# Kernel optimization log

Measured on AMD Instinct MI355X. Metric: run time of the kernel, lower is better.

The kernel has to match this reference:

```python
import jax, jax.numpy as jnp
import numpy as np

B, T, S, D = 8, 64, 256, 512


def setup_inputs() -> dict:
    key = jax.random.key(0)
    ks = jax.random.split(key, 8)
    scale = 1.0 / np.sqrt(D)
    return {
        "source": jax.random.normal(ks[0], (B, T, D), jnp.float32),
        "memory_bank": jax.random.normal(ks[1], (B, S, D), jnp.float32),
        "source_masks": jnp.ones((B, T), jnp.float32),
        # params (torch Linear stored as [out,in]; here as [in,out] so y = x @ W + b)
        "Wq": jax.random.normal(ks[2], (D, D), jnp.float32) * scale,
        "bq": jnp.zeros((D,), jnp.float32),
        "Wv": jax.random.normal(ks[3], (D, D), jnp.float32) * scale,
        "Wc": jax.random.normal(ks[4], (2 * D, 2), jnp.float32) * scale,
        "bc": jnp.zeros((2,), jnp.float32),
    }


def reference(source, memory_bank, source_masks, Wq, bq, Wv, Wc, bc):
    # accumulate(): running mean over segments == cumsum / (1..T), then mask
    counts = jnp.arange(1, T + 1, dtype=source.dtype)  # [T]
    acc = jnp.cumsum(source, axis=1) / counts[None, :, None]  # [B,T,D]
    acc = acc * source_masks[:, :, None]

    # score(): h_t = linear_query(acc); gate = v(tanh(h_t + h_s)) broadcast over (t,s)
    ht = acc @ Wq + bq  # [B,T,D]
    gate = jnp.tanh(ht[:, :, None, :] + memory_bank[:, None, :, :]) @ Wv  # [B,T,S,D]
    sum_gate = gate.sum(axis=-1)  # [B,T,S]

    # linear_cate(cat([h_s, sum_gate*h_s], -1)) split as two [D,2] matmuls;
    # sum_gate is a per-(b,t,s) scalar so (sum_gate*h_s)@Wc2 == sum_gate*(h_s@Wc2).
    part1 = memory_bank @ Wc[:D]  # [B,S,2]
    part2 = memory_bank @ Wc[D:]  # [B,S,2]
    h_fuse = part1[:, None] + sum_gate[..., None] * part2[:, None] + bc  # [B,T,S,2]
    return h_fuse
```

## Files before the change

### kernel.cpp

```cpp
#include <hip/hip_runtime.h>

constexpr int B = 8, T = 64, S = 256, D = 512;
constexpr float SCL = 2.885390081777927f;

__global__ __launch_bounds__(256) void k_prep(const float* __restrict__ src,
                                              const float* __restrict__ mask,
                                              const float* __restrict__ Wv,
                                              const float* __restrict__ Wc,
                                              const float* __restrict__ bc,
                                              const float* __restrict__ mem,
                                              float* __restrict__ acc,
                                              float* __restrict__ wv,
                                              float* __restrict__ part1,
                                              float* __restrict__ part2) {
    const int blk = blockIdx.x;
    const int tid = threadIdx.x;
    if (blk < 16) {
        int idx = blk * 256 + tid;
        int b = idx >> 9, d = idx & (D - 1);
        const float* sp = src + (size_t)b * T * D + d;
        float v[T];
#pragma unroll
        for (int t = 0; t < T; ++t) v[t] = sp[(size_t)t * D];
        const float* mp = mask + b * T;
        float* ap = acc + (size_t)b * T * D + d;
        float run = 0.f;
#pragma unroll
        for (int t = 0; t < T; ++t) {
            run += v[t];
            ap[(size_t)t * D] = run * (1.0f / (float)(t + 1)) * mp[t];
        }
    } else if (blk < 144) {
        int row = (blk - 16) * 4 + (tid >> 6);
        int lane = tid & 63;
        const float* r = Wv + (size_t)row * D;
        float s = 0.f;
#pragma unroll
        for (int j = 0; j < D / 64; ++j) s += r[lane + j * 64];
#pragma unroll
        for (int off = 32; off; off >>= 1) s += __shfl_down(s, off);
        if (lane == 0) wv[row] = s;
    } else {
        int row = (blk - 144) * 4 + (tid >> 6);
        int lane = tid & 63;
        const float* mrow = mem + (size_t)row * D;
        float a0 = 0, a1 = 0, a2 = 0, a3 = 0;
        for (int d = lane; d < D; d += 64) {
            float m = mrow[d];
            float2 w1 = *(const float2*)(Wc + d * 2);
            float2 w2 = *(const float2*)(Wc + (D + d) * 2);
            a0 = fmaf(m, w1.x, a0); a1 = fmaf(m, w1.y, a1);
            a2 = fmaf(m, w2.x, a2); a3 = fmaf(m, w2.y, a3);
        }
#pragma unroll
        for (int off = 32; off; off >>= 1) {
            a0 += __shfl_down(a0, off);
            a1 += __shfl_down(a1, off);
            a2 += __shfl_down(a2, off);
            a3 += __shfl_down(a3, off);
        }
        if (lane == 0) {
            part1[row * 2 + 0] = a0 + bc[0];
            part1[row * 2 + 1] = a1 + bc[1];
            part2[row * 2 + 0] = a2;
            part2[row * 2 + 1] = a3;
        }
    }
}

__global__ __launch_bounds__(128) void k_ht(const float* __restrict__ acc,
                                            const float* __restrict__ Wq,
                                            const float* __restrict__ bq,
                                            float* __restrict__ ht) {
    __shared__ float AL[32][34];
    __shared__ float BL[32][36];
    const int tid = threadIdx.x;
    const int r0 = blockIdx.x * 32;
    const int c0 = blockIdx.y * 32;
    const int tx = tid & 7;
    const int ty = tid >> 3;
    float s00 = 0, s01 = 0, s02 = 0, s03 = 0, s10 = 0, s11 = 0, s12 = 0, s13 = 0;
    for (int d0 = 0; d0 < D; d0 += 32) {
        __syncthreads();
#pragma unroll
        for (int k = 0; k < 2; ++k) {
            int idx = tid + k * 128;
            int row = idx >> 3;
            int c4 = (idx & 7) * 4;
            float4 va = *(const float4*)(acc + (size_t)(r0 + row) * D + d0 + c4);
            AL[c4 + 0][row] = va.x; AL[c4 + 1][row] = va.y;
            AL[c4 + 2][row] = va.z; AL[c4 + 3][row] = va.w;
            float4 vb = *(const float4*)(Wq + (size_t)(d0 + row) * D + c0 + c4);
            *(float4*)&BL[row][c4] = vb;
        }
        __syncthreads();
#pragma unroll
        for (int dd = 0; dd < 32; ++dd) {
            float2 a = *(const float2*)&AL[dd][ty * 2];
            float4 bv = *(const float4*)&BL[dd][tx * 4];
            s00 = fmaf(a.x, bv.x, s00); s01 = fmaf(a.x, bv.y, s01);
            s02 = fmaf(a.x, bv.z, s02); s03 = fmaf(a.x, bv.w, s03);
            s10 = fmaf(a.y, bv.x, s10); s11 = fmaf(a.y, bv.y, s11);
            s12 = fmaf(a.y, bv.z, s12); s13 = fmaf(a.y, bv.w, s13);
        }
    }
    int r = r0 + ty * 2, c = c0 + tx * 4;
    float4 bqv = *(const float4*)(bq + c);
    *(float4*)(ht + (size_t)r * D + c) = make_float4(
        (s00 + bqv.x) * SCL, (s01 + bqv.y) * SCL, (s02 + bqv.z) * SCL, (s03 + bqv.w) * SCL);
    *(float4*)(ht + (size_t)(r + 1) * D + c) = make_float4(
        (s10 + bqv.x) * SCL, (s11 + bqv.y) * SCL, (s12 + bqv.z) * SCL, (s13 + bqv.w) * SCL);
}

__global__ __launch_bounds__(512) void k_fusepi(const float* __restrict__ ht,
                                                const float* __restrict__ mem,
                                                const float* __restrict__ wv,
                                                const float* __restrict__ part1,
                                                const float* __restrict__ part2,
                                                float* __restrict__ out) {
    __shared__ float htT[64][17];
    __shared__ float memT[64][34];
    __shared__ float wvL[64];
    const int tid = threadIdx.x;
    const int sb = blockIdx.x;
    const int tb = blockIdx.y;
    const int b  = blockIdx.z;
    const int st = tid & 31;
    const int tt = tid >> 5;
    const float* htBase  = ht  + ((size_t)b * T + tb * 16) * D;
    const float* memBase = mem + ((size_t)b * S + sb * 32) * D;
    float a = 0.f;
#pragma unroll 1
    for (int c = 0; c < 8; ++c) {
        const int d0 = c * 64;
        __syncthreads();
        {
            int row = tid >> 4;
            int c4 = (tid & 15) * 4;
            float4 v = *(const float4*)(memBase + (size_t)row * D + d0 + c4);
            memT[c4 + 0][row] = v.x * SCL; memT[c4 + 1][row] = v.y * SCL;
            memT[c4 + 2][row] = v.z * SCL; memT[c4 + 3][row] = v.w * SCL;
        }
        if (tid < 256) {
            int row = tid >> 4;
            int c4 = (tid & 15) * 4;
            float4 v = *(const float4*)(htBase + (size_t)row * D + d0 + c4);
            htT[c4 + 0][row] = v.x; htT[c4 + 1][row] = v.y;
            htT[c4 + 2][row] = v.z; htT[c4 + 3][row] = v.w;
        } else if (tid < 272) {
            int j = tid - 256;
            float4 v = *(const float4*)(wv + d0 + j * 4);
            wvL[j * 4 + 0] = v.x; wvL[j * 4 + 1] = v.y;
            wvL[j * 4 + 2] = v.z; wvL[j * 4 + 3] = v.w;
        }
        __syncthreads();
#pragma unroll 8
        for (int dd = 0; dd < 64; ++dd) {
            float x = htT[dd][tt] + memT[dd][st];
            float e = __builtin_amdgcn_exp2f(x);
            float r = __builtin_amdgcn_rcpf(e + 1.0f);
            float th = fmaf(-2.0f, r, 1.0f);
            a = fmaf(wvL[dd], th, a);
        }
    }
    const int t = tb * 16 + tt, s = sb * 32 + st;
    float2 p1 = *(const float2*)(part1 + ((size_t)b * S + s) * 2);
    float2 p2 = *(const float2*)(part2 + ((size_t)b * S + s) * 2);
    float* o = out + (((size_t)b * T + t) * S + s) * 2;
    *(float2*)o = make_float2(p1.x + a * p2.x, p1.y + a * p2.y);
}

extern "C" void kernel_launch(void* const* d_in, const int* in_sizes, int n_in,
                              void* d_out, int out_size, void* d_ws, size_t ws_size,
                              hipStream_t stream) {
    const float* source = (const float*)d_in[0];
    const float* memory = (const float*)d_in[1];
    const float* masks  = (const float*)d_in[2];
    const float* Wq = (const float*)d_in[3];
    const float* bq = (const float*)d_in[4];
    const float* Wv = (const float*)d_in[5];
    const float* Wc = (const float*)d_in[6];
    const float* bc = (const float*)d_in[7];
    float* out = (float*)d_out;
    float* ws = (float*)d_ws;

    float* ht    = ws;
    float* accp  = ht + B * T * D;
    float* wv    = accp + B * T * D;
    float* part1 = wv + D;
    float* part2 = part1 + B * S * 2;

    k_prep<<<16 + 128 + 512, 256, 0, stream>>>(source, masks, Wv, Wc, bc, memory,
                                               accp, wv, part1, part2);
    k_ht<<<dim3(16, 16), 128, 0, stream>>>(accp, Wq, bq, ht);
    k_fusepi<<<dim3(8, 4, 8), 512, 0, stream>>>(ht, memory, wv, part1, part2, out);
}
```

Before: 117.6 us.

## Restructure pipeline: split cumsum, merge ht GEMM with prep, register-tile gate kernel

The cumsum now runs as its own kernel with more blocks, each recomputing the prefix over earlier time chunks. The Wv row sums and the memory/Wc projections are folded into the ht GEMM launch, so three launches remain. The gate kernel uses 256 threads with a 2x4 register tile per thread, splits the D reduction across waves, and combines the partials in shared memory. It also prefetches the next chunk into registers to overlap global loads with the tanh compute. This cuts LDS reads per transcendental but halves threads per block and adds a cross-wave reduction.

```diff
diff --git a/kernel.cpp b/kernel.cpp
--- a/kernel.cpp
+++ b/kernel.cpp
@@ -3,171 +3,215 @@
 constexpr int B = 8, T = 64, S = 256, D = 512;
 constexpr float SCL = 2.885390081777927f;
 
-__global__ __launch_bounds__(256) void k_prep(const float* __restrict__ src,
+__global__ __launch_bounds__(128) void k1_acc(const float* __restrict__ src,
                                               const float* __restrict__ mask,
-                                              const float* __restrict__ Wv,
-                                              const float* __restrict__ Wc,
-                                              const float* __restrict__ bc,
-                                              const float* __restrict__ mem,
-                                              float* __restrict__ acc,
-                                              float* __restrict__ wv,
-                                              float* __restrict__ part1,
-                                              float* __restrict__ part2) {
+                                              float* __restrict__ acc) {
+    int blk = blockIdx.x;
+    int b = blk >> 4, tc = (blk >> 2) & 3, dc = blk & 3;
+    int d = dc * 128 + threadIdx.x;
+    const float* sp = src + ((size_t)b * T) * D + d;
+    const float* mp = mask + b * T;
+    float* ap = acc + ((size_t)b * T) * D + d;
+    float run = 0.f;
+    for (int ch = 0; ch <= tc; ++ch) {
+        float v[16];
+#pragma unroll
+        for (int i = 0; i < 16; ++i) v[i] = sp[(size_t)(ch * 16 + i) * D];
+        if (ch < tc) {
+#pragma unroll
+            for (int i = 0; i < 16; ++i) run += v[i];
+        } else {
+#pragma unroll
+            for (int i = 0; i < 16; ++i) {
+                run += v[i];
+                int t = ch * 16 + i;
+                ap[(size_t)t * D] = run * __builtin_amdgcn_rcpf((float)(t + 1)) * mp[t];
+            }
+        }
+    }
+}
+
+__global__ __launch_bounds__(128) void k2_htwp(const float* __restrict__ acc,
+                                               const float* __restrict__ Wq,
+                                               const float* __restrict__ bq,
+                                               const float* __restrict__ Wv,
+                                               const float* __restrict__ mem,
+                                               const float* __restrict__ Wc,
+                                               const float* __restrict__ bc,
+                                               float* __restrict__ ht,
+                                               float* __restrict__ wv,
+                                               float* __restrict__ part1,
+                                               float* __restrict__ part2) {
     const int blk = blockIdx.x;
     const int tid = threadIdx.x;
-    if (blk < 16) {
-        int idx = blk * 256 + tid;
-        int b = idx >> 9, d = idx & (D - 1);
-        const float* sp = src + (size_t)b * T * D + d;
-        float v[T];
-#pragma unroll
-        for (int t = 0; t < T; ++t) v[t] = sp[(size_t)t * D];
-        const float* mp = mask + b * T;
-        float* ap = acc + (size_t)b * T * D + d;
-        float run = 0.f;
-#pragma unroll
-        for (int t = 0; t < T; ++t) {
-            run += v[t];
-            ap[(size_t)t * D] = run * (1.0f / (float)(t + 1)) * mp[t];
-        }
-    } else if (blk < 144) {
-        int row = (blk - 16) * 4 + (tid >> 6);
-        int lane = tid & 63;
-        const float* r = Wv + (size_t)row * D;
-        float s = 0.f;
-#pragma unroll
-        for (int j = 0; j < D / 64; ++j) s += r[lane + j * 64];
-#pragma unroll
-        for (int off = 32; off; off >>= 1) s += __shfl_down(s, off);
-        if (lane == 0) wv[row] = s;
+    if (blk < 256) {
+        __shared__ float AL[32][34];
+        __shared__ float BL[32][36];
+        const int r0 = (blk >> 4) * 32;
+        const int c0 = (blk & 15) * 32;
+        const int tx = tid & 7, ty = tid >> 3;
+        float s00 = 0, s01 = 0, s02 = 0, s03 = 0, s10 = 0, s11 = 0, s12 = 0, s13 = 0;
+        for (int d0 = 0; d0 < D; d0 += 32) {
+            __syncthreads();
+#pragma unroll
+            for (int k = 0; k < 2; ++k) {
+                int idx = tid + k * 128;
+                int row = idx >> 3;
+                int c4 = (idx & 7) * 4;
+                float4 va = *(const float4*)(acc + (size_t)(r0 + row) * D + d0 + c4);
+                AL[c4 + 0][row] = va.x; AL[c4 + 1][row] = va.y;
+                AL[c4 + 2][row] = va.z; AL[c4 + 3][row] = va.w;
+                float4 vb = *(const float4*)(Wq + (size_t)(d0 + row) * D + c0 + c4);
+                *(float4*)&BL[row][c4] = vb;
+            }
+            __syncthreads();
+#pragma unroll
+            for (int dd = 0; dd < 32; ++dd) {
+                float2 a = *(const float2*)&AL[dd][ty * 2];
+                float4 bv = *(const float4*)&BL[dd][tx * 4];
+                s00 = fmaf(a.x, bv.x, s00); s01 = fmaf(a.x, bv.y, s01);
+                s02 = fmaf(a.x, bv.z, s02); s03 = fmaf(a.x, bv.w, s03);
+                s10 = fmaf(a.y, bv.x, s10); s11 = fmaf(a.y, bv.y, s11);
+                s12 = fmaf(a.y, bv.z, s12); s13 = fmaf(a.y, bv.w, s13);
+            }
+        }
+        int r = r0 + ty * 2, c = c0 + tx * 4;
+        float4 bqv = *(const float4*)(bq + c);
+        *(float4*)(ht + (size_t)r * D + c) = make_float4(
+            (s00 + bqv.x) * SCL, (s01 + bqv.y) * SCL, (s02 + bqv.z) * SCL, (s03 + bqv.w) * SCL);
+        *(float4*)(ht + (size_t)(r + 1) * D + c) = make_float4(
+            (s10 + bqv.x) * SCL, (s11 + bqv.y) * SCL, (s12 + bqv.z) * SCL, (s13 + bqv.w) * SCL);
+    } else if (blk < 288) {
+        int w = tid >> 6, lane = tid & 63;
+        int base = (blk - 256) * 16 + w * 8;
+        for (int it = 0; it < 8; ++it) {
+            int row = base + it;
+            const float* r = Wv + (size_t)row * D;
+            float s = 0.f;
+#pragma unroll
+            for (int j = 0; j < D / 64; ++j) s += r[lane + j * 64];
+#pragma unroll
+            for (int off = 32; off; off >>= 1) s += __shfl_down(s, off);
+            if (lane == 0) wv[row] = s;
+        }
     } else {
-        int row = (blk - 144) * 4 + (tid >> 6);
-        int lane = tid & 63;
-        const float* mrow = mem + (size_t)row * D;
-        float a0 = 0, a1 = 0, a2 = 0, a3 = 0;
-        for (int d = lane; d < D; d += 64) {
-            float m = mrow[d];
-            float2 w1 = *(const float2*)(Wc + d * 2);
-            float2 w2 = *(const float2*)(Wc + (D + d) * 2);
-            a0 = fmaf(m, w1.x, a0); a1 = fmaf(m, w1.y, a1);
-            a2 = fmaf(m, w2.x, a2); a3 = fmaf(m, w2.y, a3);
-        }
-#pragma unroll
-        for (int off = 32; off; off >>= 1) {
-            a0 += __shfl_down(a0, off);
-            a1 += __shfl_down(a1, off);
-            a2 += __shfl_down(a2, off);
-            a3 += __shfl_down(a3, off);
-        }
-        if (lane == 0) {
-            part1[row * 2 + 0] = a0 + bc[0];
-            part1[row * 2 + 1] = a1 + bc[1];
-            part2[row * 2 + 0] = a2;
-            part2[row * 2 + 1] = a3;
+        int w = tid >> 6, lane = tid & 63;
+        int base = (blk - 288) * 16 + w * 8;
+        for (int it = 0; it < 8; ++it) {
+            int row = base + it;
+            const float* mrow = mem + (size_t)row * D;
+            float a0 = 0, a1 = 0, a2 = 0, a3 = 0;
+#pragma unroll
+            for (int j = 0; j < D / 64; ++j) {
+                int d = lane + j * 64;
+                float m = mrow[d];
+                float2 w1 = *(const float2*)(Wc + d * 2);
+                float2 w2 = *(const float2*)(Wc + (D + d) * 2);
+                a0 = fmaf(m, w1.x, a0); a1 = fmaf(m, w1.y, a1);
+                a2 = fmaf(m, w2.x, a2); a3 = fmaf(m, w2.y, a3);
+            }
+#pragma unroll
+            for (int off = 32; off; off >>= 1) {
+                a0 += __shfl_down(a0, off);
+                a1 += __shfl_down(a1, off);
+                a2 += __shfl_down(a2, off);
+                a3 += __shfl_down(a3, off);
+            }
+            if (lane == 0) {
+                part1[row * 2 + 0] = a0 + bc[0];
+                part1[row * 2 + 1] = a1 + bc[1];
+                part2[row * 2 + 0] = a2;
+                part2[row * 2 + 1] = a3;
+            }
         }
     }
 }
 
-__global__ __launch_bounds__(128) void k_ht(const float* __restrict__ acc,
-                                            const float* __restrict__ Wq,
-                                            const float* __restrict__ bq,
-                                            float* __restrict__ ht) {
-    __shared__ float AL[32][34];
-    __shared__ float BL[32][36];
+__global__ __launch_bounds__(256) void k3_gate(const float* __restrict__ ht,
+                                               const float* __restrict__ mem,
+                                               const float* __restrict__ wv,
+                                               const float* __restrict__ part1,
+                                               const float* __restrict__ part2,
+                                               float* __restrict__ out) {
+    __shared__ float htT[64][18];
+    __shared__ float memT[64][36];
+    __shared__ float wvL[64];
+    __shared__ float pt[4][16][33];
     const int tid = threadIdx.x;
-    const int r0 = blockIdx.x * 32;
-    const int c0 = blockIdx.y * 32;
-    const int tx = tid & 7;
-    const int ty = tid >> 3;
-    float s00 = 0, s01 = 0, s02 = 0, s03 = 0, s10 = 0, s11 = 0, s12 = 0, s13 = 0;
-    for (int d0 = 0; d0 < D; d0 += 32) {
-        __syncthreads();
-#pragma unroll
-        for (int k = 0; k < 2; ++k) {
-            int idx = tid + k * 128;
-            int row = idx >> 3;
-            int c4 = (idx & 7) * 4;
-            float4 va = *(const float4*)(acc + (size_t)(r0 + row) * D + d0 + c4);
-            AL[c4 + 0][row] = va.x; AL[c4 + 1][row] = va.y;
-            AL[c4 + 2][row] = va.z; AL[c4 + 3][row] = va.w;
-            float4 vb = *(const float4*)(Wq + (size_t)(d0 + row) * D + c0 + c4);
-            *(float4*)&BL[row][c4] = vb;
-        }
-        __syncthreads();
-#pragma unroll
-        for (int dd = 0; dd < 32; ++dd) {
-            float2 a = *(const float2*)&AL[dd][ty * 2];
-            float4 bv = *(const float4*)&BL[dd][tx * 4];
-            s00 = fmaf(a.x, bv.x, s00); s01 = fmaf(a.x, bv.y, s01);
-            s02 = fmaf(a.x, bv.z, s02); s03 = fmaf(a.x, bv.w, s03);
-            s10 = fmaf(a.y, bv.x, s10); s11 = fmaf(a.y, bv.y, s11);
-            s12 = fmaf(a.y, bv.z, s12); s13 = fmaf(a.y, bv.w, s13);
-        }
-    }
-    int r = r0 + ty * 2, c = c0 + tx * 4;
-    float4 bqv = *(const float4*)(bq + c);
-    *(float4*)(ht + (size_t)r * D + c) = make_float4(
-        (s00 + bqv.x) * SCL, (s01 + bqv.y) * SCL, (s02 + bqv.z) * SCL, (s03 + bqv.w) * SCL);
-    *(float4*)(ht + (size_t)(r + 1) * D + c) = make_float4(
-        (s10 + bqv.x) * SCL, (s11 + bqv.y) * SCL, (s12 + bqv.z) * SCL, (s13 + bqv.w) * SCL);
-}
-
-__global__ __launch_bounds__(512) void k_fusepi(const float* __restrict__ ht,
-                                                const float* __restrict__ mem,
-                                                const float* __restrict__ wv,
-                                                const float* __restrict__ part1,
-                                                const float* __restrict__ part2,
-                                                float* __restrict__ out) {
-    __shared__ float htT[64][17];
-    __shared__ float memT[64][34];
-    __shared__ float wvL[64];
-    const int tid = threadIdx.x;
-    const int sb = blockIdx.x;
-    const int tb = blockIdx.y;
-    const int b  = blockIdx.z;
-    const int st = tid & 31;
-    const int tt = tid >> 5;
-    const float* htBase  = ht  + ((size_t)b * T + tb * 16) * D;
+    const int sb = blockIdx.x, tb = blockIdx.y, b = blockIdx.z;
+    const int lane = tid & 63, w = tid >> 6;
+    const int ss = lane & 7, tt = lane >> 3;
+    const float* htBase = ht + ((size_t)b * T + tb * 16) * D;
     const float* memBase = mem + ((size_t)b * S + sb * 32) * D;
-    float a = 0.f;
+    const int hrow = tid >> 4;
+    const int c4 = (tid & 15) * 4;
+    const int mrow1 = hrow + 16;
+    float4 ph = *(const float4*)(htBase + (size_t)hrow * D + c4);
+    float4 pm0 = *(const float4*)(memBase + (size_t)hrow * D + c4);
+    float4 pm1 = *(const float4*)(memBase + (size_t)mrow1 * D + c4);
+    float4 pw;
+    if (tid < 16) pw = *(const float4*)(wv + tid * 4);
+    float a[2][4];
+#pragma unroll
+    for (int r = 0; r < 2; ++r)
+#pragma unroll
+        for (int j = 0; j < 4; ++j) a[r][j] = 0.f;
 #pragma unroll 1
     for (int c = 0; c < 8; ++c) {
-        const int d0 = c * 64;
         __syncthreads();
-        {
-            int row = tid >> 4;
-            int c4 = (tid & 15) * 4;
-            float4 v = *(const float4*)(memBase + (size_t)row * D + d0 + c4);
-            memT[c4 + 0][row] = v.x * SCL; memT[c4 + 1][row] = v.y * SCL;
-            memT[c4 + 2][row] = v.z * SCL; memT[c4 + 3][row] = v.w * SCL;
-        }
-        if (tid < 256) {
-            int row = tid >> 4;
-            int c4 = (tid & 15) * 4;
-            float4 v = *(const float4*)(htBase + (size_t)row * D + d0 + c4);
-            htT[c4 + 0][row] = v.x; htT[c4 + 1][row] = v.y;
-            htT[c4 + 2][row] = v.z; htT[c4 + 3][row] = v.w;
-        } else if (tid < 272) {
-            int j = tid - 256;
-            float4 v = *(const float4*)(wv + d0 + j * 4);
-            wvL[j * 4 + 0] = v.x; wvL[j * 4 + 1] = v.y;
-            wvL[j * 4 + 2] = v.z; wvL[j * 4 + 3] = v.w;
+        htT[c4 + 0][hrow] = ph.x; htT[c4 + 1][hrow] = ph.y;
+        htT[c4 + 2][hrow] = ph.z; htT[c4 + 3][hrow] = ph.w;
+        memT[c4 + 0][hrow] = pm0.x * SCL; memT[c4 + 1][hrow] = pm0.y * SCL;
+        memT[c4 + 2][hrow] = pm0.z * SCL; memT[c4 + 3][hrow] = pm0.w * SCL;
+        memT[c4 + 0][mrow1] = pm1.x * SCL; memT[c4 + 1][mrow1] = pm1.y * SCL;
+        memT[c4 + 2][mrow1] = pm1.z * SCL; memT[c4 + 3][mrow1] = pm1.w * SCL;
+        if (tid < 16) {
+            wvL[tid * 4 + 0] = pw.x; wvL[tid * 4 + 1] = pw.y;
+            wvL[tid * 4 + 2] = pw.z; wvL[tid * 4 + 3] = pw.w;
         }
         __syncthreads();
-#pragma unroll 8
-        for (int dd = 0; dd < 64; ++dd) {
-            float x = htT[dd][tt] + memT[dd][st];
-            float e = __builtin_amdgcn_exp2f(x);
-            float r = __builtin_amdgcn_rcpf(e + 1.0f);
-            float th = fmaf(-2.0f, r, 1.0f);
-            a = fmaf(wvL[dd], th, a);
+        if (c < 7) {
+            int d0 = (c + 1) * 64;
+            ph = *(const float4*)(htBase + (size_t)hrow * D + d0 + c4);
+            pm0 = *(const float4*)(memBase + (size_t)hrow * D + d0 + c4);
+            pm1 = *(const float4*)(memBase + (size_t)mrow1 * D + d0 + c4);
+            if (tid < 16) pw = *(const float4*)(wv + d0 + tid * 4);
+        }
+        const int dbase = w * 16;
+#pragma unroll
+        for (int i = 0; i < 16; ++i) {
+            int dd = dbase + i;
+            float2 h2 = *(const float2*)&htT[dd][tt * 2];
+            float4 m4 = *(const float4*)&memT[dd][ss * 4];
+            float wvv = wvL[dd];
+            float hs[2] = {h2.x, h2.y};
+            float ms[4] = {m4.x, m4.y, m4.z, m4.w};
+#pragma unroll
+            for (int r = 0; r < 2; ++r)
+#pragma unroll
+                for (int j = 0; j < 4; ++j) {
+                    float e = __builtin_amdgcn_exp2f(hs[r] + ms[j]);
+                    float th = fmaf(-2.0f, __builtin_amdgcn_rcpf(e + 1.0f), 1.0f);
+                    a[r][j] = fmaf(wvv, th, a[r][j]);
+                }
         }
     }
-    const int t = tb * 16 + tt, s = sb * 32 + st;
-    float2 p1 = *(const float2*)(part1 + ((size_t)b * S + s) * 2);
-    float2 p2 = *(const float2*)(part2 + ((size_t)b * S + s) * 2);
-    float* o = out + (((size_t)b * T + t) * S + s) * 2;
-    *(float2*)o = make_float2(p1.x + a * p2.x, p1.y + a * p2.y);
+    __syncthreads();
+#pragma unroll
+    for (int r = 0; r < 2; ++r)
+#pragma unroll
+        for (int j = 0; j < 4; ++j) pt[w][tt * 2 + r][ss * 4 + j] = a[r][j];
+    __syncthreads();
+    const int t = tid >> 4;
+    const int s0 = (tid & 15) * 2;
+    float sg0 = pt[0][t][s0] + pt[1][t][s0] + pt[2][t][s0] + pt[3][t][s0];
+    float sg1 = pt[0][t][s0 + 1] + pt[1][t][s0 + 1] + pt[2][t][s0 + 1] + pt[3][t][s0 + 1];
+    const int srow = b * S + sb * 32 + s0;
+    float4 p1 = *(const float4*)(part1 + (size_t)srow * 2);
+    float4 p2 = *(const float4*)(part2 + (size_t)srow * 2);
+    float* o = out + (((size_t)b * T + tb * 16 + t) * S + sb * 32 + s0) * 2;
+    *(float4*)o = make_float4(p1.x + sg0 * p2.x, p1.y + sg0 * p2.y,
+                              p1.z + sg1 * p2.z, p1.w + sg1 * p2.w);
 }
 
 extern "C" void kernel_launch(void* const* d_in, const int* in_sizes, int n_in,
@@ -184,14 +228,14 @@
     float* out = (float*)d_out;
     float* ws = (float*)d_ws;
 
-    float* ht    = ws;
-    float* accp  = ht + B * T * D;
-    float* wv    = accp + B * T * D;
+    float* accp  = ws;
+    float* ht    = accp + B * T * D;
+    float* wv    = ht + B * T * D;
     float* part1 = wv + D;
     float* part2 = part1 + B * S * 2;
 
-    k_prep<<<16 + 128 + 512, 256, 0, stream>>>(source, masks, Wv, Wc, bc, memory,
-                                               accp, wv, part1, part2);
-    k_ht<<<dim3(16, 16), 128, 0, stream>>>(accp, Wq, bq, ht);
-    k_fusepi<<<dim3(8, 4, 8), 512, 0, stream>>>(ht, memory, wv, part1, part2, out);
-}
+    k1_acc<<<128, 128, 0, stream>>>(source, masks, accp);
+    k2_htwp<<<416, 128, 0, stream>>>(accp, Wq, bq, Wv, memory, Wc, bc,
+                                     ht, wv, part1, part2);
+    k3_gate<<<dim3(8, 4, 8), 256, 0, stream>>>(ht, memory, wv, part1, part2, out);
+}
```

Measured after the change: 111.8 us. 4.9% less time.
